# Kernel optimization log

Hardware: AMD Instinct MI355X
Metric: run time of the kernel (lower is better)

The kernel has to match this reference:

```python
import jax, jax.numpy as jnp
import numpy as np

NUM_HEADS = 8
NUM_GROUPS = 32
EPS = 1e-5


def group_norm(x, gamma, beta):
    b, c, h, w = x.shape
    xg = x.reshape(b, NUM_GROUPS, c // NUM_GROUPS, h, w)
    mean = jnp.mean(xg, axis=(2, 3, 4), keepdims=True)
    var = jnp.var(xg, axis=(2, 3, 4), keepdims=True)
    xn = ((xg - mean) * jax.lax.rsqrt(var + EPS)).reshape(b, c, h, w)
    return xn * gamma[None, :, None, None] + beta[None, :, None, None]


def setup_inputs() -> dict:
    key = jax.random.key(0)
    ks = jax.random.split(key, 4)
    b, c, h, w = 16, 512, 32, 32
    x = jax.random.normal(ks[0], (b, c, h, w), dtype=jnp.float32)
    gn_gamma = jnp.ones((c,), dtype=jnp.float32)
    gn_beta = jnp.zeros((c,), dtype=jnp.float32)
    qkv_w = jax.random.normal(ks[1], (3 * c, c), dtype=jnp.float32) * (1.0 / np.sqrt(c))
    qkv_b = jnp.zeros((3 * c,), dtype=jnp.float32)
    proj_w = jax.random.normal(ks[2], (c, c), dtype=jnp.float32) * (1.0 / np.sqrt(c))
    proj_b = jnp.zeros((c,), dtype=jnp.float32)
    return {"x": x, "gn_gamma": gn_gamma, "gn_beta": gn_beta,
            "qkv_w": qkv_w, "qkv_b": qkv_b, "proj_w": proj_w, "proj_b": proj_b}


def reference(x, gn_gamma, gn_beta, qkv_w, qkv_b, proj_w, proj_b):
    b, c, h, w = x.shape
    hd = c // NUM_HEADS
    hw = h * w

    xn = group_norm(x, gn_gamma, gn_beta)
    # 1x1 conv == channel matmul
    qkv = jnp.einsum('oc,bchw->bohw', qkv_w, xn) + qkv_b[None, :, None, None]
    q, k, v = jnp.split(qkv, 3, axis=1)
    q = q.reshape(b, NUM_HEADS, hd, hw)
    k = k.reshape(b, NUM_HEADS, hd, hw)
    v = v.reshape(b, NUM_HEADS, hd, hw)

    scale = 1.0 / np.sqrt(hd)
    attn = jnp.einsum('bhdt,bhds->bhts', q, k) * scale  # [b,H,hw,hw]
    attn = jax.nn.softmax(attn, axis=-1)
    h_attn = jnp.einsum('bhts,bhds->bhdt', attn, v).reshape(b, c, h, w)

    h_attn = jnp.einsum('oc,bchw->bohw', proj_w, h_attn) + proj_b[None, :, None, None]
    return x + h_attn
```

## Files before the change

kernel.cpp:

```cpp
#include <hip/hip_runtime.h>
#include <math.h>

#define NUM_HEADS 8
#define NUM_GROUPS 32
#define EPS 1e-5f

constexpr int B  = 16;
constexpr int C  = 512;
constexpr int HW = 1024;
constexpr int HD = 64;

typedef short bf16x8 __attribute__((ext_vector_type(8)));
typedef float f32x4  __attribute__((ext_vector_type(4)));

#define QSCALE 0.1803368801111f

__device__ inline unsigned short f2bf(float f) {
    union { float f; unsigned int u; } v; v.f = f;
    unsigned int r = (v.u + 0x7FFFu + ((v.u >> 16) & 1u)) >> 16;
    return (unsigned short)r;
}

__device__ __forceinline__ void gld_lds16(void* lds, const void* g) {
    __builtin_amdgcn_global_load_lds(
        (const __attribute__((address_space(1))) void*)g,
        (__attribute__((address_space(3))) void*)lds, 16, 0, 0);
}

__global__ __launch_bounds__(256)
void groupnorm_t_kernel(const float* __restrict__ x,
                        const float* __restrict__ gamma,
                        const float* __restrict__ beta,
                        unsigned short* __restrict__ xnT) {
    const int bg = blockIdx.x;
    const int b = bg >> 5, g = bg & 31;
    const size_t base = ((size_t)b * C + (size_t)g * 16) * HW;
    const float4* xp4 = (const float4*)(x + base);

    float sum = 0.f, sumsq = 0.f;
    for (int i = threadIdx.x; i < 4096; i += 256) {
        float4 v = xp4[i];
        sum += v.x + v.y + v.z + v.w;
        sumsq += v.x * v.x + v.y * v.y + v.z * v.z + v.w * v.w;
    }
    #pragma unroll
    for (int off = 32; off > 0; off >>= 1) {
        sum   += __shfl_down(sum, off, 64);
        sumsq += __shfl_down(sumsq, off, 64);
    }
    __shared__ float s_sum[4], s_sq[4];
    const int wid = threadIdx.x >> 6, lane = threadIdx.x & 63;
    if (lane == 0) { s_sum[wid] = sum; s_sq[wid] = sumsq; }
    __syncthreads();
    const float tsum = s_sum[0] + s_sum[1] + s_sum[2] + s_sum[3];
    const float tsq  = s_sq[0] + s_sq[1] + s_sq[2] + s_sq[3];
    const float mean = tsum * (1.0f / 16384.f);
    const float var  = tsq * (1.0f / 16384.f) - mean * mean;
    const float rstd = rsqrtf(var + EPS);

    float ga[16], be[16];
    #pragma unroll
    for (int cl = 0; cl < 16; ++cl) {
        ga[cl] = gamma[g * 16 + cl] * rstd;
        be[cl] = beta[g * 16 + cl] - mean * ga[cl];
    }

    #pragma unroll
    for (int p = 0; p < 4; ++p) {
        const int t = threadIdx.x + p * 256;
        unsigned short pk[16];
        #pragma unroll
        for (int cl = 0; cl < 16; ++cl) {
            const float v = x[base + (size_t)cl * HW + t];
            pk[cl] = f2bf(v * ga[cl] + be[cl]);
        }
        unsigned short* dst = xnT + ((size_t)(b * 1024 + t)) * 512 + g * 16;
        *(uint4*)dst = *(const uint4*)pk;
        *(uint4*)(dst + 8) = *(const uint4*)(pk + 8);
    }
}

__global__ __launch_bounds__(256)
void wconv_kernel(const float* __restrict__ qkv_w,
                  const float* __restrict__ proj_w,
                  unsigned short* __restrict__ wqb) {
    const int i = blockIdx.x * 256 + threadIdx.x;
    const int n1 = 786432 / 4;
    const int nt = 1048576 / 4;
    if (i >= nt) return;
    const float4 v = (i < n1) ? ((const float4*)qkv_w)[i]
                              : ((const float4*)proj_w)[i - n1];
    ushort4 r;
    r.x = f2bf(v.x); r.y = f2bf(v.y); r.z = f2bf(v.z); r.w = f2bf(v.w);
    ((ushort4*)wqb)[i] = r;
}

__device__ __forceinline__ void mfma_gemm_core(const char* __restrict__ Ab,
                                               const char* __restrict__ Bb,
                                               unsigned short* As,
                                               unsigned short* Bs,
                                               f32x4 acc[4][4]) {
    const int tid = threadIdx.x;
    const int w = tid >> 6, lane = tid & 63;
    const int lo = lane & 15, q4 = lane >> 4;
    const int wm = w >> 1, wn = w & 1;
    const int lrow = lane >> 2, lkc = lane & 3;

    for (int k0 = 0; k0 < 512; k0 += 32) {
        __syncthreads();
        #pragma unroll
        for (int i = 0; i < 2; ++i) {
            const int row = w * 32 + i * 16 + lrow;
            const int kc = lkc ^ ((row >> 1) & 3);
            const size_t goff = (size_t)row * 1024 + k0 * 2 + kc * 16;
            gld_lds16((char*)As + w * 2048 + i * 1024, Ab + goff);
            gld_lds16((char*)Bs + w * 2048 + i * 1024, Bb + goff);
        }
        __syncthreads();

        bf16x8 af[4], bfr[4];
        #pragma unroll
        for (int i = 0; i < 4; ++i) {
            const int ra = wm * 64 + i * 16 + lo;
            af[i]  = *(const bf16x8*)(As + ra * 32 + (q4 ^ ((ra >> 1) & 3)) * 8);
            const int rb = wn * 64 + i * 16 + lo;
            bfr[i] = *(const bf16x8*)(Bs + rb * 32 + (q4 ^ ((rb >> 1) & 3)) * 8);
        }
        #pragma unroll
        for (int mi = 0; mi < 4; ++mi)
            #pragma unroll
            for (int ni = 0; ni < 4; ++ni)
                acc[mi][ni] = __builtin_amdgcn_mfma_f32_16x16x32_bf16(
                    af[mi], bfr[ni], acc[mi][ni], 0, 0, 0);
    }
}

__global__ __launch_bounds__(256)
void qkv_mfma_kernel(const unsigned short* __restrict__ wqb,
                     const unsigned short* __restrict__ xnT,
                     const float* __restrict__ qkv_b,
                     unsigned short* __restrict__ Qt,
                     unsigned short* __restrict__ Kt,
                     unsigned short* __restrict__ Vb) {
    __shared__ __align__(16) unsigned short As[128 * 32];
    __shared__ __align__(16) unsigned short Bs[128 * 32];
    const int batch = blockIdx.z;
    const int mBase = blockIdx.y * 128, nBase = blockIdx.x * 128;

    f32x4 acc[4][4] = {};
    mfma_gemm_core((const char*)(wqb + (size_t)mBase * 512),
                   (const char*)(xnT + ((size_t)batch * 1024 + nBase) * 512),
                   As, Bs, acc);

    const int tid = threadIdx.x;
    const int w = tid >> 6, lane = tid & 63;
    const int lo = lane & 15, q4 = lane >> 4;
    const int wm = w >> 1, wn = w & 1;
    const int mw = mBase + wm * 64;
    const int tb = nBase + wn * 64;

    if (mw < 1024) {
        const bool isQ = mw < 512;
        const int head = (mw >> 6) & 7;
        unsigned short* dst = (isQ ? Qt : Kt) + (((size_t)batch * 8 + head) << 16);
        const float sc = isQ ? QSCALE : 1.0f;
        #pragma unroll
        for (int mi = 0; mi < 4; ++mi) {
            const float4 bq = *(const float4*)(qkv_b + mw + mi * 16 + q4 * 4);
            #pragma unroll
            for (int ni = 0; ni < 4; ++ni) {
                const int t = tb + ni * 16 + lo;
                ushort4 pk;
                pk.x = f2bf((acc[mi][ni][0] + bq.x) * sc);
                pk.y = f2bf((acc[mi][ni][1] + bq.y) * sc);
                pk.z = f2bf((acc[mi][ni][2] + bq.z) * sc);
                pk.w = f2bf((acc[mi][ni][3] + bq.w) * sc);
                *(ushort4*)(dst + (size_t)t * 64 + mi * 16 + q4 * 4) = pk;
            }
        }
    } else {
        unsigned short* dst = Vb + (size_t)batch * 524288 + (size_t)(mw - 1024) * 1024;
        #pragma unroll
        for (int mi = 0; mi < 4; ++mi) {
            const float4 bq = *(const float4*)(qkv_b + mw + mi * 16 + q4 * 4);
            #pragma unroll
            for (int ni = 0; ni < 4; ++ni) {
                const int t = tb + ni * 16 + lo;
                dst[(size_t)(mi * 16 + q4 * 4 + 0) * 1024 + t] = f2bf(acc[mi][ni][0] + bq.x);
                dst[(size_t)(mi * 16 + q4 * 4 + 1) * 1024 + t] = f2bf(acc[mi][ni][1] + bq.y);
                dst[(size_t)(mi * 16 + q4 * 4 + 2) * 1024 + t] = f2bf(acc[mi][ni][2] + bq.z);
                dst[(size_t)(mi * 16 + q4 * 4 + 3) * 1024 + t] = f2bf(acc[mi][ni][3] + bq.w);
            }
        }
    }
}

__global__ __launch_bounds__(256, 2)
void attn_mfma_kernel(const unsigned short* __restrict__ Qt,
                      const unsigned short* __restrict__ Kt,
                      const unsigned short* __restrict__ Vb,
                      unsigned short* __restrict__ attnT) {
    const int bh = blockIdx.x;
    const int b = bh >> 3, h = bh & 7;
    const int tBase = blockIdx.y * 256;
    const int tid = threadIdx.x;
    const int w = tid >> 6, lane = tid & 63;
    const int lo = lane & 15, q4 = lane >> 4;
    const int xr = lo & 7;

    __shared__ __align__(16) unsigned short Ks[2][64 * 64];
    __shared__ __align__(16) unsigned short Vs[2][64 * 64];
    __shared__ __align__(16) unsigned short Ps[4][64 * 64];

    const unsigned short* Kp = Kt + ((size_t)bh << 16);
    const unsigned short* Vp = Vb + ((size_t)b * 512 + h * 64) * 1024;

    bf16x8 qf[4][2];
    {
        const unsigned short* Qp = Qt + ((size_t)bh * 1024 + tBase + 64 * w) * 64;
        #pragma unroll
        for (int nt = 0; nt < 4; ++nt) {
            qf[nt][0] = *(const bf16x8*)(Qp + (size_t)(16 * nt + lo) * 64 + 8 * q4);
            qf[nt][1] = *(const bf16x8*)(Qp + (size_t)(16 * nt + lo) * 64 + 32 + 8 * q4);
        }
    }

    const int rl = lane >> 3, p8 = lane & 7;
    auto stage = [&](unsigned short* Kd, unsigned short* Vd, int s0) {
        #pragma unroll
        for (int cc = 0; cc < 2; ++cc) {
            const int r = 16 * w + 8 * cc + rl;
            const int j = p8 ^ (r & 7);
            gld_lds16(Kd + (16 * w + 8 * cc) * 64, Kp + (size_t)(s0 + r) * 64 + j * 8);
            gld_lds16(Vd + (16 * w + 8 * cc) * 64, Vp + (size_t)r * 1024 + s0 + j * 8);
        }
    };

    f32x4 oacc[4][4] = {};
    float lrun[4] = {0.f, 0.f, 0.f, 0.f};
    unsigned short* Pw = Ps[w];

    stage(Ks[0], Vs[0], 0);

    for (int i = 0; i < 16; ++i) {
        __syncthreads();
        if (i < 15) stage(Ks[(i + 1) & 1], Vs[(i + 1) & 1], (i + 1) * 64);
        const unsigned short* Kcur = Ks[i & 1];
        const unsigned short* Vcur = Vs[i & 1];

        f32x4 sacc[4][4] = {};
        #pragma unroll
        for (int mt = 0; mt < 4; ++mt) {
            const unsigned short* kr = Kcur + (16 * mt + lo) * 64;
            const bf16x8 a0 = *(const bf16x8*)(kr + ((q4    ) ^ xr) * 8);
            const bf16x8 a1 = *(const bf16x8*)(kr + ((q4 + 4) ^ xr) * 8);
            #pragma unroll
            for (int nt = 0; nt < 4; ++nt) {
                sacc[mt][nt] = __builtin_amdgcn_mfma_f32_16x16x32_bf16(a0, qf[nt][0], sacc[mt][nt], 0, 0, 0);
                sacc[mt][nt] = __builtin_amdgcn_mfma_f32_16x16x32_bf16(a1, qf[nt][1], sacc[mt][nt], 0, 0, 0);
            }
        }

        #pragma unroll
        for (int nt = 0; nt < 4; ++nt) {
            float ps = 0.f;
            const int t = 16 * nt + lo;
            #pragma unroll
            for (int mt = 0; mt < 4; ++mt) {
                const f32x4 s = sacc[mt][nt];
                const float p0 = exp2f(s[0]);
                const float p1 = exp2f(s[1]);
                const float p2 = exp2f(s[2]);
                const float p3 = exp2f(s[3]);
                ps += (p0 + p1) + (p2 + p3);
                ushort4 pk;
                pk.x = f2bf(p0); pk.y = f2bf(p1); pk.z = f2bf(p2); pk.w = f2bf(p3);
                const int sc = 2 * mt + (q4 >> 1);
                *(ushort4*)(Pw + t * 64 + ((sc ^ xr) * 8) + 4 * (q4 & 1)) = pk;
            }
            lrun[nt] += ps;
        }

        bf16x8 bp[4][2];
        #pragma unroll
        for (int nt = 0; nt < 4; ++nt) {
            const unsigned short* pr = Pw + (16 * nt + lo) * 64;
            bp[nt][0] = *(const bf16x8*)(pr + ((q4    ) ^ xr) * 8);
            bp[nt][1] = *(const bf16x8*)(pr + ((q4 + 4) ^ xr) * 8);
        }
        #pragma unroll
        for (int mt = 0; mt < 4; ++mt) {
            const unsigned short* vr = Vcur + (16 * mt + lo) * 64;
            const bf16x8 v0 = *(const bf16x8*)(vr + ((q4    ) ^ xr) * 8);
            const bf16x8 v1 = *(const bf16x8*)(vr + ((q4 + 4) ^ xr) * 8);
            #pragma unroll
            for (int nt = 0; nt < 4; ++nt) {
                oacc[mt][nt] = __builtin_amdgcn_mfma_f32_16x16x32_bf16(v0, bp[nt][0], oacc[mt][nt], 0, 0, 0);
                oacc[mt][nt] = __builtin_amdgcn_mfma_f32_16x16x32_bf16(v1, bp[nt][1], oacc[mt][nt], 0, 0, 0);
            }
        }
    }

    #pragma unroll
    for (int nt = 0; nt < 4; ++nt) {
        float lt = lrun[nt];
        lt += __shfl_xor(lt, 16, 64);
        lt += __shfl_xor(lt, 32, 64);
        const float inv = 1.0f / lt;
        const int t = tBase + 64 * w + 16 * nt + lo;
        unsigned short* op = attnT + ((size_t)(b * 1024 + t)) * 512 + h * 64;
        #pragma unroll
        for (int mt = 0; mt < 4; ++mt) {
            ushort4 pk;
            pk.x = f2bf(oacc[mt][nt][0] * inv);
            pk.y = f2bf(oacc[mt][nt][1] * inv);
            pk.z = f2bf(oacc[mt][nt][2] * inv);
            pk.w = f2bf(oacc[mt][nt][3] * inv);
            *(ushort4*)(op + 16 * mt + 4 * q4) = pk;
        }
    }
}

__global__ __launch_bounds__(256)
void proj_mfma_kernel(const unsigned short* __restrict__ wpb,
                      const unsigned short* __restrict__ attnT,
                      const float* __restrict__ proj_b,
                      const float* __restrict__ x,
                      float* __restrict__ out) {
    __shared__ __align__(16) unsigned short As[128 * 32];
    __shared__ __align__(16) unsigned short Bs[128 * 32];
    const int batch = blockIdx.z;
    const int mBase = blockIdx.y * 128, nBase = blockIdx.x * 128;

    f32x4 acc[4][4] = {};
    mfma_gemm_core((const char*)(wpb + (size_t)mBase * 512),
                   (const char*)(attnT + ((size_t)batch * 1024 + nBase) * 512),
                   As, Bs, acc);

    const int tid = threadIdx.x;
    const int w = tid >> 6, lane = tid & 63;
    const int lo = lane & 15, q4 = lane >> 4;
    const int wm = w >> 1, wn = w & 1;
    const float* xb = x + (size_t)batch * 524288;
    float* ob = out + (size_t)batch * 524288;

    #pragma unroll
    for (int mi = 0; mi < 4; ++mi) {
        const int m0 = mBase + wm * 64 + mi * 16 + q4 * 4;
        const float4 bq = *(const float4*)(proj_b + m0);
        #pragma unroll
        for (int ni = 0; ni < 4; ++ni) {
            const int t = nBase + wn * 64 + ni * 16 + lo;
            const size_t o0 = (size_t)m0 * 1024 + t;
            ob[o0]          = acc[mi][ni][0] + bq.x + xb[o0];
            ob[o0 + 1024]   = acc[mi][ni][1] + bq.y + xb[o0 + 1024];
            ob[o0 + 2048]   = acc[mi][ni][2] + bq.z + xb[o0 + 2048];
            ob[o0 + 3072]   = acc[mi][ni][3] + bq.w + xb[o0 + 3072];
        }
    }
}

extern "C" void kernel_launch(void* const* d_in, const int* in_sizes, int n_in,
                              void* d_out, int out_size, void* d_ws, size_t ws_size,
                              hipStream_t stream) {
    const float* x        = (const float*)d_in[0];
    const float* gn_gamma = (const float*)d_in[1];
    const float* gn_beta  = (const float*)d_in[2];
    const float* qkv_w    = (const float*)d_in[3];
    const float* qkv_b    = (const float*)d_in[4];
    const float* proj_w   = (const float*)d_in[5];
    const float* proj_b   = (const float*)d_in[6];
    float* out = (float*)d_out;

    char* wsc = (char*)d_ws;
    unsigned short* xnT   = (unsigned short*)(wsc);
    unsigned short* Qt    = (unsigned short*)(wsc + 16777216);
    unsigned short* Kt    = (unsigned short*)(wsc + 33554432);
    unsigned short* Vb    = (unsigned short*)(wsc + 50331648);
    unsigned short* attnT = (unsigned short*)(wsc + 67108864);
    unsigned short* wqb   = (unsigned short*)(wsc + 83886080);
    unsigned short* wpb   = wqb + 786432;

    groupnorm_t_kernel<<<B * NUM_GROUPS, 256, 0, stream>>>(x, gn_gamma, gn_beta, xnT);

    wconv_kernel<<<1024, 256, 0, stream>>>(qkv_w, proj_w, wqb);

    {
        dim3 grid(HW / 128, (3 * C) / 128, B);
        qkv_mfma_kernel<<<grid, 256, 0, stream>>>(wqb, xnT, qkv_b, Qt, Kt, Vb);
    }

    {
        dim3 grid(B * NUM_HEADS, HW / 256);
        attn_mfma_kernel<<<grid, 256, 0, stream>>>(Qt, Kt, Vb, attnT);
    }

    {
        dim3 grid(HW / 128, C / 128, B);
        proj_mfma_kernel<<<grid, 256, 0, stream>>>(wpb, attnT, proj_b, x, out);
    }
}
```

Before: 248.0 us.

## Cache groupnorm inputs in registers, stage V stores via LDS, truncate bf16 packs

Groupnorm now keeps each thread's 64 input values in registers, so x is read from global memory once instead of twice. The V epilogue of the QKV GEMM transposes through shared memory and writes 16-byte coalesced rows, replacing scattered 2-byte global stores. In the attention kernel, the P tile and the output conversion to bf16 use a single byte-permute truncation instead of round-to-nearest-even, which cuts ALU work but adds a small rounding bias.

```diff
diff --git a/kernel.cpp b/kernel.cpp
--- a/kernel.cpp
+++ b/kernel.cpp
@@ -19,6 +19,10 @@
     union { float f; unsigned int u; } v; v.f = f;
     unsigned int r = (v.u + 0x7FFFu + ((v.u >> 16) & 1u)) >> 16;
     return (unsigned short)r;
+}
+
+__device__ __forceinline__ unsigned int pack_trunc(float lo, float hi) {
+    return __builtin_amdgcn_perm(__float_as_uint(hi), __float_as_uint(lo), 0x07060302u);
 }
 
 __device__ __forceinline__ void gld_lds16(void* lds, const void* g) {
@@ -35,13 +39,19 @@
     const int bg = blockIdx.x;
     const int b = bg >> 5, g = bg & 31;
     const size_t base = ((size_t)b * C + (size_t)g * 16) * HW;
-    const float4* xp4 = (const float4*)(x + base);
-
+
+    float v[4][16];
     float sum = 0.f, sumsq = 0.f;
-    for (int i = threadIdx.x; i < 4096; i += 256) {
-        float4 v = xp4[i];
-        sum += v.x + v.y + v.z + v.w;
-        sumsq += v.x * v.x + v.y * v.y + v.z * v.z + v.w * v.w;
+    #pragma unroll
+    for (int p = 0; p < 4; ++p) {
+        const int t = threadIdx.x + p * 256;
+        #pragma unroll
+        for (int cl = 0; cl < 16; ++cl) {
+            const float f = x[base + (size_t)cl * HW + t];
+            v[p][cl] = f;
+            sum += f;
+            sumsq += f * f;
+        }
     }
     #pragma unroll
     for (int off = 32; off > 0; off >>= 1) {
@@ -70,10 +80,8 @@
         const int t = threadIdx.x + p * 256;
         unsigned short pk[16];
         #pragma unroll
-        for (int cl = 0; cl < 16; ++cl) {
-            const float v = x[base + (size_t)cl * HW + t];
-            pk[cl] = f2bf(v * ga[cl] + be[cl]);
-        }
+        for (int cl = 0; cl < 16; ++cl)
+            pk[cl] = f2bf(v[p][cl] * ga[cl] + be[cl]);
         unsigned short* dst = xnT + ((size_t)(b * 1024 + t)) * 512 + g * 16;
         *(uint4*)dst = *(const uint4*)pk;
         *(uint4*)(dst + 8) = *(const uint4*)(pk + 8);
@@ -142,8 +150,9 @@
                      unsigned short* __restrict__ Qt,
                      unsigned short* __restrict__ Kt,
                      unsigned short* __restrict__ Vb) {
-    __shared__ __align__(16) unsigned short As[128 * 32];
-    __shared__ __align__(16) unsigned short Bs[128 * 32];
+    __shared__ __align__(16) unsigned short SMEM[8192];
+    unsigned short* As = SMEM;
+    unsigned short* Bs = SMEM + 4096;
     const int batch = blockIdx.z;
     const int mBase = blockIdx.y * 128, nBase = blockIdx.x * 128;
 
@@ -158,6 +167,8 @@
     const int wm = w >> 1, wn = w & 1;
     const int mw = mBase + wm * 64;
     const int tb = nBase + wn * 64;
+
+    __syncthreads();
 
     if (mw < 1024) {
         const bool isQ = mw < 512;
@@ -179,17 +190,30 @@
             }
         }
     } else {
-        unsigned short* dst = Vb + (size_t)batch * 524288 + (size_t)(mw - 1024) * 1024;
-        #pragma unroll
-        for (int mi = 0; mi < 4; ++mi) {
-            const float4 bq = *(const float4*)(qkv_b + mw + mi * 16 + q4 * 4);
-            #pragma unroll
-            for (int ni = 0; ni < 4; ++ni) {
-                const int t = tb + ni * 16 + lo;
-                dst[(size_t)(mi * 16 + q4 * 4 + 0) * 1024 + t] = f2bf(acc[mi][ni][0] + bq.x);
-                dst[(size_t)(mi * 16 + q4 * 4 + 1) * 1024 + t] = f2bf(acc[mi][ni][1] + bq.y);
-                dst[(size_t)(mi * 16 + q4 * 4 + 2) * 1024 + t] = f2bf(acc[mi][ni][2] + bq.z);
-                dst[(size_t)(mi * 16 + q4 * 4 + 3) * 1024 + t] = f2bf(acc[mi][ni][3] + bq.w);
+        unsigned short* T = SMEM + w * 2048;
+        unsigned short* Vrow = Vb + (size_t)batch * 524288 + (size_t)(mw - 1024) * 1024 + tb;
+        const int rl8 = lane >> 3, c8 = lane & 7;
+        #pragma unroll
+        for (int p = 0; p < 2; ++p) {
+            #pragma unroll
+            for (int mi2 = 0; mi2 < 2; ++mi2) {
+                const int mi = 2 * p + mi2;
+                const float4 bq = *(const float4*)(qkv_b + mw + mi * 16 + q4 * 4);
+                const int dl = mi2 * 16 + q4 * 4;
+                #pragma unroll
+                for (int ni = 0; ni < 4; ++ni) {
+                    const int tl = ni * 16 + lo;
+                    T[(dl + 0) * 64 + tl] = f2bf(acc[mi][ni][0] + bq.x);
+                    T[(dl + 1) * 64 + tl] = f2bf(acc[mi][ni][1] + bq.y);
+                    T[(dl + 2) * 64 + tl] = f2bf(acc[mi][ni][2] + bq.z);
+                    T[(dl + 3) * 64 + tl] = f2bf(acc[mi][ni][3] + bq.w);
+                }
+            }
+            #pragma unroll
+            for (int i = 0; i < 4; ++i) {
+                const int dl = i * 8 + rl8;
+                const uint4 val = *(const uint4*)&T[dl * 64 + c8 * 8];
+                *(uint4*)(Vrow + (size_t)(p * 32 + dl) * 1024 + c8 * 8) = val;
             }
         }
     }
@@ -273,10 +297,11 @@
                 const float p2 = exp2f(s[2]);
                 const float p3 = exp2f(s[3]);
                 ps += (p0 + p1) + (p2 + p3);
-                ushort4 pk;
-                pk.x = f2bf(p0); pk.y = f2bf(p1); pk.z = f2bf(p2); pk.w = f2bf(p3);
+                uint2 pk;
+                pk.x = pack_trunc(p0, p1);
+                pk.y = pack_trunc(p2, p3);
                 const int sc = 2 * mt + (q4 >> 1);
-                *(ushort4*)(Pw + t * 64 + ((sc ^ xr) * 8) + 4 * (q4 & 1)) = pk;
+                *(uint2*)(Pw + t * 64 + ((sc ^ xr) * 8) + 4 * (q4 & 1)) = pk;
             }
             lrun[nt] += ps;
         }
@@ -311,12 +336,10 @@
         unsigned short* op = attnT + ((size_t)(b * 1024 + t)) * 512 + h * 64;
         #pragma unroll
         for (int mt = 0; mt < 4; ++mt) {
-            ushort4 pk;
-            pk.x = f2bf(oacc[mt][nt][0] * inv);
-            pk.y = f2bf(oacc[mt][nt][1] * inv);
-            pk.z = f2bf(oacc[mt][nt][2] * inv);
-            pk.w = f2bf(oacc[mt][nt][3] * inv);
-            *(ushort4*)(op + 16 * mt + 4 * q4) = pk;
+            uint2 pk;
+            pk.x = pack_trunc(oacc[mt][nt][0] * inv, oacc[mt][nt][1] * inv);
+            pk.y = pack_trunc(oacc[mt][nt][2] * inv, oacc[mt][nt][3] * inv);
+            *(uint2*)(op + 16 * mt + 4 * q4) = pk;
         }
     }
 }
```

Result: faster. 239.0 us (-3.6%).
